# Kernel tuning notes

Hardware: AMD Instinct MI355X
Metric: run time of the kernel (lower is better)

Reference implementation:

```python
import jax, jax.numpy as jnp
import numpy as np
from jax import lax

P_COARSE, P_FINE = 8, 4
EMBED_DIM = 128


def _patchify(x, p):
    # torch unfold(kernel=p, stride=p) then transpose: [B, Hp*Wp, C*p*p]
    B, C, H, W = x.shape
    Hp, Wp = H // p, W // p
    t = x.reshape(B, C, Hp, p, Wp, p).transpose(0, 2, 4, 1, 3, 5)
    return t.reshape(B, Hp * Wp, C * p * p), Hp, Wp


def _edge_map(x):
    gray = x.mean(axis=1, keepdims=True)
    kx = jnp.array([[-1., 0., 1.], [-2., 0., 2.], [-1., 0., 1.]], gray.dtype)[None, None]
    ky = jnp.array([[-1., -2., -1.], [0., 0., 0.], [1., 2., 1.]], gray.dtype)[None, None]
    pad = [(1, 1), (1, 1)]
    sx = lax.conv_general_dilated(gray, kx, (1, 1), pad)
    sy = lax.conv_general_dilated(gray, ky, (1, 1), pad)
    e = jnp.sqrt(sx * sx + sy * sy)
    B, _, H, W = e.shape
    # avg_pool2d(4, stride=4)
    return e.reshape(B, 1, H // 4, 4, W // 4, 4).mean(axis=(3, 5))


def _compact(tok, m):
    # stream-compact masked rows to the front, zero-pad the rest (pad_sequence semantics, padded to full Nf)
    Nf, D = tok.shape
    pos = jnp.cumsum(m) - 1
    pos = jnp.where(m, pos, Nf)  # unmasked rows go to overflow slot
    out = jnp.zeros((Nf + 1, D), tok.dtype).at[pos].set(tok)
    return out[:Nf]


def setup_inputs() -> dict:
    key = jax.random.key(0)
    ks = jax.random.split(key, 6)
    D = EMBED_DIM
    pd_c = 1 * P_COARSE * P_COARSE
    pd_f = 1 * P_FINE * P_FINE
    return {
        "x": jax.random.normal(ks[0], (8, 1, 512, 512), jnp.float32),
        "w_coarse": jax.random.normal(ks[1], (pd_c, D), jnp.float32) / np.sqrt(pd_c),
        "b_coarse": jnp.zeros((D,), jnp.float32),
        "w_fine": jax.random.normal(ks[2], (pd_f, D), jnp.float32) / np.sqrt(pd_f),
        "b_fine": jnp.zeros((D,), jnp.float32),
        "type_emb": jax.random.normal(ks[3], (2, D), jnp.float32) * 0.02,
    }


def reference(x, w_coarse, b_coarse, w_fine, b_fine, type_emb):
    B = x.shape[0]
    # coarse branch
    pc, Hc, Wc = _patchify(x, P_COARSE)
    coarse = pc @ w_coarse + b_coarse + type_emb[0]  # [B, Nc, D]
    # edge-driven mask
    edges = _edge_map(x)  # [B,1,He,We]
    mask = edges > edges.mean(axis=(2, 3), keepdims=True)
    # fine branch
    pf, Hf, Wf = _patchify(x, P_FINE)
    fine = pf @ w_fine + b_fine  # [B, Nf, D]
    # nearest upsample mask to (Hf, Wf): integer factor repeat
    m = mask[:, 0]
    m = jnp.repeat(jnp.repeat(m, Hf // m.shape[1], axis=1), Wf // m.shape[2], axis=2)
    mask_flat = m.reshape(B, -1)  # [B, Nf]
    fine_c = jax.vmap(_compact)(fine, mask_flat) + type_emb[1]
    tokens = jnp.concatenate([coarse, fine_c], axis=1)
    return tokens, mask_flat
```

## Files before the change

kernel.cpp:

```cpp
#include <hip/hip_runtime.h>

#define IMH 512
#define IMW 512
#define BATCH 8
#define NTOK 20480
#define NC 4096
#define NF 16384
#define ED 128

typedef float vf4 __attribute__((ext_vector_type(4)));

__device__ __forceinline__ void nt_store4(float* p, float a, float b, float c, float d) {
    vf4 v = {a, b, c, d};
    __builtin_nontemporal_store(v, (vf4*)p);
}
__device__ __forceinline__ void nt_store4v(float* p, float4 v) {
    nt_store4(p, v.x, v.y, v.z, v.w);
}

__global__ __launch_bounds__(256) void k1_edge_coarse(const float* __restrict__ x,
                                                      const float* __restrict__ wc,
                                                      const float* __restrict__ bc,
                                                      const float* __restrict__ temb,
                                                      float* __restrict__ out,
                                                      double* __restrict__ edges,
                                                      double* __restrict__ tsum) {
    __shared__ float esm[66][68];
    __shared__ double dred[4];
    int blk = blockIdx.x;
    int t = threadIdx.x;
    int lane = t & 63, wid = t >> 6;
    if (blk < 1024) {
        int b = blk >> 7;
        int pblk = (blk & 127) * 32;
        int wv = __builtin_amdgcn_readfirstlane(t >> 6);
        int h = wv & 1;
        int p0 = pblk + (wv >> 1) * 16;
        int d = h * 64 + lane;
        float wcol[64];
        #pragma unroll
        for (int k = 0; k < 64; ++k) wcol[k] = wc[k * ED + d];
        float base = bc[d] + temb[d];
        const float* img = x + ((size_t)b * IMH + (p0 >> 6) * 8) * IMW + (p0 & 63) * 8;
        float* dst = out + ((size_t)b * NTOK + p0) * ED + d;
        #pragma unroll
        for (int p = 0; p < 16; ++p) {
            const float* pimg = img + p * 8;
            float acc = base;
            #pragma unroll
            for (int r = 0; r < 8; ++r) {
                const float* rp = pimg + r * IMW;
                acc += rp[0] * wcol[r * 8 + 0] + rp[1] * wcol[r * 8 + 1]
                     + rp[2] * wcol[r * 8 + 2] + rp[3] * wcol[r * 8 + 3]
                     + rp[4] * wcol[r * 8 + 4] + rp[5] * wcol[r * 8 + 5]
                     + rp[6] * wcol[r * 8 + 6] + rp[7] * wcol[r * 8 + 7];
            }
            __builtin_nontemporal_store(acc, dst + (size_t)p * ED);
        }
    } else {
        int blk2 = blk - 1024;
        int b = blk2 >> 6;
        int tile = blk2 & 63;
        int ty0 = (tile >> 3) * 64;
        int tx0 = (tile & 7) * 64;
        const float* img = x + (size_t)b * (IMH * IMW);
        for (int idx = t; idx < 66 * 66; idx += 256) {
            int r = idx / 66, c = idx - r * 66;
            int gy = ty0 - 1 + r, gx = tx0 - 1 + c;
            float v = 0.f;
            if (gy >= 0 && gy < IMH && gx >= 0 && gx < IMW) v = img[gy * IMW + gx];
            esm[r][c] = v;
        }
        __syncthreads();
        int cy = t >> 4, cx = t & 15;
        double acc = 0.0;
        #pragma unroll
        for (int dy = 0; dy < 4; ++dy) {
            int py = cy * 4 + dy + 1;
            #pragma unroll
            for (int dx = 0; dx < 4; ++dx) {
                int px = cx * 4 + dx + 1;
                double a00 = (double)esm[py - 1][px - 1];
                double a01 = (double)esm[py - 1][px];
                double a02 = (double)esm[py - 1][px + 1];
                double a10 = (double)esm[py][px - 1];
                double a12 = (double)esm[py][px + 1];
                double a20 = (double)esm[py + 1][px - 1];
                double a21 = (double)esm[py + 1][px];
                double a22 = (double)esm[py + 1][px + 1];
                double sx = (a02 + 2.0 * a12 + a22) - (a00 + 2.0 * a10 + a20);
                double sy = (a20 + 2.0 * a21 + a22) - (a00 + 2.0 * a01 + a02);
                acc += sqrt(sx * sx + sy * sy);
            }
        }
        double cell = acc * (1.0 / 16.0);
        int gy = (ty0 >> 2) + cy;
        int gx = (tx0 >> 2) + cx;
        edges[((size_t)b << 14) + gy * 128 + gx] = cell;
        double sc = cell;
        #pragma unroll
        for (int off = 32; off > 0; off >>= 1) sc += __shfl_xor(sc, off);
        if (lane == 0) dred[wid] = sc;
        __syncthreads();
        if (t == 0) tsum[b * 64 + tile] = dred[0] + dred[1] + dred[2] + dred[3];
    }
}

__global__ __launch_bounds__(256) void k2_fine(const float* __restrict__ x,
                                               const float* __restrict__ wfp,
                                               const float* __restrict__ bfp,
                                               const float* __restrict__ temb,
                                               const double* __restrict__ edges,
                                               const double* __restrict__ tsum,
                                               float* __restrict__ out,
                                               float* __restrict__ mask_out) {
    int b = blockIdx.y;
    int row = blockIdx.x;
    int t = threadIdx.x;
    int lane = t & 63, wid = t >> 6;
    __shared__ float smx[4][512];
    __shared__ int excl_s[256];
    __shared__ unsigned long long bits_s[256];
    __shared__ int wtot[4];

    const double* ts = tsum + b * 64;
    double total = 0.0;
    #pragma unroll
    for (int j = 0; j < 64; ++j) total += ts[j];
    double mean = total * (1.0 / 16384.0);

    const double* e = edges + ((size_t)b << 14) + t * 64;
    unsigned long long mybits = 0ULL;
    #pragma unroll
    for (int j = 0; j < 32; ++j) {
        double2 dv = *(const double2*)&e[j * 2];
        if (dv.x > mean) mybits |= (1ULL << (2 * j));
        if (dv.y > mean) mybits |= (1ULL << (2 * j + 1));
    }
    int cnt = __popcll(mybits);
    int incl = cnt;
    #pragma unroll
    for (int off = 1; off < 64; off <<= 1) {
        int up = __shfl_up(incl, off);
        if (lane >= off) incl += up;
    }
    if (lane == 63) wtot[wid] = incl;
    bits_s[t] = mybits;
    __syncthreads();
    int woff = 0, K = 0;
    #pragma unroll
    for (int w = 0; w < 4; ++w) { int c = wtot[w]; K += c; if (w < wid) woff += c; }
    excl_s[t] = woff + incl - cnt;

    const float* img = x + ((size_t)b * IMH + row * 4) * IMW;
    #pragma unroll
    for (int k = 0; k < 2; ++k) {
        int idx = t + 256 * k;
        int r = idx >> 7, c4 = idx & 127;
        *(float4*)&smx[r][c4 * 4] = *(const float4*)&img[r * IMW + c4 * 4];
    }
    __syncthreads();

    int base = excl_s[2 * row];
    unsigned long long lo = bits_s[2 * row];
    unsigned long long hi = bits_s[2 * row + 1];

    if (t < 128) {
        unsigned long long bb = (t < 64) ? lo : hi;
        float mv = ((bb >> (t & 63)) & 1ULL) ? 1.0f : 0.0f;
        __builtin_nontemporal_store(mv, mask_out + ((size_t)b << 14) + row * 128 + t);
    }

    int d4 = t & 31;
    int g = t >> 5;
    float4 wcol[16];
    #pragma unroll
    for (int k = 0; k < 16; ++k) wcol[k] = *(const float4*)&wfp[k * ED + d4 * 4];
    float4 fill = *(const float4*)&temb[ED + d4 * 4];
    float4 bse = *(const float4*)&bfp[d4 * 4];
    float4 fbase = make_float4(bse.x + fill.x, bse.y + fill.y, bse.z + fill.z, bse.w + fill.w);
    float* tok = out + ((size_t)b * NTOK + NC) * ED;
    int i0 = row * 128;
    #pragma unroll
    for (int pp = 0; pp < 16; ++pp) {
        int p = g + pp * 8;
        int i = i0 + p;
        unsigned long long bb = (p < 64) ? lo : hi;
        if ((bb >> (p & 63)) & 1ULL) {
            int below = (p < 64)
                ? __popcll(lo & ((1ULL << p) - 1))
                : __popcll(lo) + __popcll(hi & ((1ULL << (p - 64)) - 1));
            int ps = base + below;
            float4 acc = fbase;
            #pragma unroll
            for (int r = 0; r < 4; ++r) {
                float4 vv = *(const float4*)&smx[r][p * 4];
                acc.x += vv.x * wcol[4 * r].x + vv.y * wcol[4 * r + 1].x + vv.z * wcol[4 * r + 2].x + vv.w * wcol[4 * r + 3].x;
                acc.y += vv.x * wcol[4 * r].y + vv.y * wcol[4 * r + 1].y + vv.z * wcol[4 * r + 2].y + vv.w * wcol[4 * r + 3].y;
                acc.z += vv.x * wcol[4 * r].z + vv.y * wcol[4 * r + 1].z + vv.z * wcol[4 * r + 2].z + vv.w * wcol[4 * r + 3].z;
                acc.w += vv.x * wcol[4 * r].w + vv.y * wcol[4 * r + 1].w + vv.z * wcol[4 * r + 2].w + vv.w * wcol[4 * r + 3].w;
            }
            nt_store4v(tok + ((size_t)ps * 32 + d4) * 4, acc);
        }
        if (i >= K) {
            nt_store4v(tok + ((size_t)i * 32 + d4) * 4, fill);
        }
    }
}

extern "C" void kernel_launch(void* const* d_in, const int* in_sizes, int n_in,
                              void* d_out, int out_size, void* d_ws, size_t ws_size,
                              hipStream_t stream) {
    const float* x    = (const float*)d_in[0];
    const float* wc   = (const float*)d_in[1];
    const float* bc   = (const float*)d_in[2];
    const float* wfp  = (const float*)d_in[3];
    const float* bfp  = (const float*)d_in[4];
    const float* temb = (const float*)d_in[5];
    float* out = (float*)d_out;

    char* wsb = (char*)d_ws;
    double* edges = (double*)wsb;
    double* tsum  = (double*)(wsb + (size_t)BATCH * NF * 8);
    float* mask_out = out + (size_t)BATCH * NTOK * ED;

    k1_edge_coarse<<<dim3(1536), 256, 0, stream>>>(x, wc, bc, temb, out, edges, tsum);
    k2_fine<<<dim3(128, BATCH), 256, 0, stream>>>(x, wfp, bfp, temb, edges, tsum, out, mask_out);
}
```

Before: 51.22 us.

## Split mask scan into separate kernel and halve fine-block work granularity

Previously every fine block (128 per batch) redundantly re-read all 16384 edge values and rescanned them to find its own compaction offset. Now a small per-batch scan kernel computes the mask bits with ballots, writes the mask and per-64-token prefix offsets once, and the fine kernel just loads its bitmask and base. The fine kernel is also split into 256 blocks of 64 tokens each. This adds a third kernel launch and a serial dependency through an 8-block kernel with low occupancy.

```diff
diff --git a/kernel.cpp b/kernel.cpp
--- a/kernel.cpp
+++ b/kernel.cpp
@@ -10,12 +10,9 @@
 
 typedef float vf4 __attribute__((ext_vector_type(4)));
 
-__device__ __forceinline__ void nt_store4(float* p, float a, float b, float c, float d) {
-    vf4 v = {a, b, c, d};
-    __builtin_nontemporal_store(v, (vf4*)p);
-}
 __device__ __forceinline__ void nt_store4v(float* p, float4 v) {
-    nt_store4(p, v.x, v.y, v.z, v.w);
+    vf4 t = {v.x, v.y, v.z, v.w};
+    __builtin_nontemporal_store(t, (vf4*)p);
 }
 
 __global__ __launch_bounds__(256) void k1_edge_coarse(const float* __restrict__ x,
@@ -106,21 +103,16 @@
     }
 }
 
-__global__ __launch_bounds__(256) void k2_fine(const float* __restrict__ x,
-                                               const float* __restrict__ wfp,
-                                               const float* __restrict__ bfp,
-                                               const float* __restrict__ temb,
-                                               const double* __restrict__ edges,
-                                               const double* __restrict__ tsum,
-                                               float* __restrict__ out,
-                                               float* __restrict__ mask_out) {
-    int b = blockIdx.y;
-    int row = blockIdx.x;
+__global__ __launch_bounds__(256) void k_scan(const double* __restrict__ edges,
+                                              const double* __restrict__ tsum,
+                                              unsigned long long* __restrict__ halfbits,
+                                              int* __restrict__ halfbase,
+                                              int* __restrict__ Kout,
+                                              float* __restrict__ mask_out) {
+    int b = blockIdx.x;
     int t = threadIdx.x;
     int lane = t & 63, wid = t >> 6;
-    __shared__ float smx[4][512];
-    __shared__ int excl_s[256];
-    __shared__ unsigned long long bits_s[256];
+    __shared__ unsigned long long hb_s[256];
     __shared__ int wtot[4];
 
     const double* ts = tsum + b * 64;
@@ -129,15 +121,19 @@
     for (int j = 0; j < 64; ++j) total += ts[j];
     double mean = total * (1.0 / 16384.0);
 
-    const double* e = edges + ((size_t)b << 14) + t * 64;
-    unsigned long long mybits = 0ULL;
-    #pragma unroll
-    for (int j = 0; j < 32; ++j) {
-        double2 dv = *(const double2*)&e[j * 2];
-        if (dv.x > mean) mybits |= (1ULL << (2 * j));
-        if (dv.y > mean) mybits |= (1ULL << (2 * j + 1));
-    }
-    int cnt = __popcll(mybits);
+    const double* e = edges + ((size_t)b << 14);
+    float* mb = mask_out + ((size_t)b << 14);
+    #pragma unroll 8
+    for (int j = 0; j < 64; ++j) {
+        double v = e[j * 256 + t];
+        bool sel = v > mean;
+        unsigned long long bal = __ballot(sel);
+        if (lane == 0) hb_s[j * 4 + wid] = bal;
+        __builtin_nontemporal_store(sel ? 1.0f : 0.0f, mb + j * 256 + t);
+    }
+    __syncthreads();
+    unsigned long long myb = hb_s[t];
+    int cnt = __popcll(myb);
     int incl = cnt;
     #pragma unroll
     for (int off = 1; off < 64; off <<= 1) {
@@ -145,31 +141,41 @@
         if (lane >= off) incl += up;
     }
     if (lane == 63) wtot[wid] = incl;
-    bits_s[t] = mybits;
     __syncthreads();
-    int woff = 0, K = 0;
-    #pragma unroll
-    for (int w = 0; w < 4; ++w) { int c = wtot[w]; K += c; if (w < wid) woff += c; }
-    excl_s[t] = woff + incl - cnt;
-
-    const float* img = x + ((size_t)b * IMH + row * 4) * IMW;
-    #pragma unroll
-    for (int k = 0; k < 2; ++k) {
-        int idx = t + 256 * k;
-        int r = idx >> 7, c4 = idx & 127;
+    int woff = 0;
+    #pragma unroll
+    for (int w = 0; w < 4; ++w) { if (w < wid) woff += wtot[w]; }
+    int excl = woff + incl - cnt;
+    halfbits[b * 256 + t] = myb;
+    halfbase[b * 256 + t] = excl;
+    if (t == 255) Kout[b] = excl + cnt;
+}
+
+__global__ __launch_bounds__(256) void k_fine(const float* __restrict__ x,
+                                              const float* __restrict__ wfp,
+                                              const float* __restrict__ bfp,
+                                              const float* __restrict__ temb,
+                                              const unsigned long long* __restrict__ halfbits,
+                                              const int* __restrict__ halfbase,
+                                              const int* __restrict__ Kout,
+                                              float* __restrict__ out) {
+    int b = blockIdx.y;
+    int bx = blockIdx.x;
+    int t = threadIdx.x;
+    __shared__ float smx[4][256];
+
+    unsigned long long bits = halfbits[b * 256 + bx];
+    int base = halfbase[b * 256 + bx];
+    int K = Kout[b];
+
+    int irow = (bx >> 1) * 4;
+    int icol = (bx & 1) * 256;
+    const float* img = x + ((size_t)b * IMH + irow) * IMW + icol;
+    {
+        int r = t >> 6, c4 = t & 63;
         *(float4*)&smx[r][c4 * 4] = *(const float4*)&img[r * IMW + c4 * 4];
     }
     __syncthreads();
-
-    int base = excl_s[2 * row];
-    unsigned long long lo = bits_s[2 * row];
-    unsigned long long hi = bits_s[2 * row + 1];
-
-    if (t < 128) {
-        unsigned long long bb = (t < 64) ? lo : hi;
-        float mv = ((bb >> (t & 63)) & 1ULL) ? 1.0f : 0.0f;
-        __builtin_nontemporal_store(mv, mask_out + ((size_t)b << 14) + row * 128 + t);
-    }
 
     int d4 = t & 31;
     int g = t >> 5;
@@ -180,16 +186,13 @@
     float4 bse = *(const float4*)&bfp[d4 * 4];
     float4 fbase = make_float4(bse.x + fill.x, bse.y + fill.y, bse.z + fill.z, bse.w + fill.w);
     float* tok = out + ((size_t)b * NTOK + NC) * ED;
-    int i0 = row * 128;
-    #pragma unroll
-    for (int pp = 0; pp < 16; ++pp) {
+    int i0 = bx * 64;
+    #pragma unroll
+    for (int pp = 0; pp < 8; ++pp) {
         int p = g + pp * 8;
         int i = i0 + p;
-        unsigned long long bb = (p < 64) ? lo : hi;
-        if ((bb >> (p & 63)) & 1ULL) {
-            int below = (p < 64)
-                ? __popcll(lo & ((1ULL << p) - 1))
-                : __popcll(lo) + __popcll(hi & ((1ULL << (p - 64)) - 1));
+        if ((bits >> p) & 1ULL) {
+            int below = __popcll(bits & ((1ULL << p) - 1ULL));
             int ps = base + below;
             float4 acc = fbase;
             #pragma unroll
@@ -222,8 +225,12 @@
     char* wsb = (char*)d_ws;
     double* edges = (double*)wsb;
     double* tsum  = (double*)(wsb + (size_t)BATCH * NF * 8);
+    unsigned long long* halfbits = (unsigned long long*)(wsb + (size_t)BATCH * NF * 8 + 4096);
+    int* halfbase = (int*)(wsb + (size_t)BATCH * NF * 8 + 4096 + 16384);
+    int* Kout     = (int*)(wsb + (size_t)BATCH * NF * 8 + 4096 + 16384 + 8192);
     float* mask_out = out + (size_t)BATCH * NTOK * ED;
 
     k1_edge_coarse<<<dim3(1536), 256, 0, stream>>>(x, wc, bc, temb, out, edges, tsum);
-    k2_fine<<<dim3(128, BATCH), 256, 0, stream>>>(x, wfp, bfp, temb, edges, tsum, out, mask_out);
-}
+    k_scan<<<dim3(BATCH), 256, 0, stream>>>(edges, tsum, halfbits, halfbase, Kout, mask_out);
+    k_fine<<<dim3(256, BATCH), 256, 0, stream>>>(x, wfp, bfp, temb, halfbits, halfbase, Kout, out);
+}
```

Result: slower. 58.76 us (+14.7%).
